# Performance work log

Measured on AMD Instinct MI355X. Metric: run time of the kernel, lower is better.

Reference implementation:

```python
import jax, jax.numpy as jnp
import numpy as np

EPS = 1e-8


def _entropy_1d(p):
    # entropy() helper with input_as_probabilities=True on a 1-D tensor:
    # clamp to EPS, x*log(x), return -sum
    p_ = jnp.maximum(p, EPS)
    return -jnp.sum(p_ * jnp.log(p_))


def setup_inputs() -> dict:
    key = jax.random.key(0)
    k1, k2 = jax.random.split(key)
    b, n = 65536, 512
    anchors = jax.random.normal(k1, (b, n), dtype=jnp.float32)
    neighbors = jax.random.normal(k2, (b, n), dtype=jnp.float32)
    return {"anchors": anchors, "neighbors": neighbors}


def reference(anchors, neighbors):
    entropy_weight = 2.0
    b, n = anchors.shape

    anchors_prob = jax.nn.softmax(anchors, axis=1)      # [b, n]
    positives_prob = jax.nn.softmax(neighbors, axis=1)  # [b, n]

    # bmm of [b,1,n] x [b,n,1] -> row-wise dot product, shape [b]
    similarity = jnp.einsum('bn,bn->b', anchors_prob, positives_prob)

    # BCELoss(similarity, ones) = -mean(log(sim)); torch clamps log at -100
    consistency_loss = -jnp.mean(jnp.maximum(jnp.log(similarity), -100.0))

    lg_sim = jnp.log(similarity)

    entropy_loss = _entropy_1d(jnp.mean(anchors_prob, axis=0))

    # cross/second-order: dot of clamped sim with clamped log-sim
    second_order_loss = jnp.dot(jnp.maximum(similarity, EPS),
                                jnp.maximum(lg_sim, EPS))

    # np.tile(sim, n).reshape(n, b) then view(b, n, 1): equivalent to the
    # flat [b*n] tiled vector reshaped row-major to [b, n]
    tiled_sim = jnp.tile(similarity, n).reshape(b, n)
    third_order_entropy = jnp.einsum('bn,bn->b', anchors_prob, tiled_sim)
    lg_third = jnp.log(third_order_entropy)
    third_order_loss = jnp.dot(jnp.maximum(third_order_entropy, EPS),
                               jnp.maximum(lg_third, EPS)) / n

    third_weight = 0.5 / np.sqrt(n)
    diff_weight = 0.25 / n

    total_loss = (consistency_loss
                  - entropy_weight * entropy_loss
                  + diff_weight * second_order_loss
                  - third_weight * third_order_loss)
    return (total_loss, consistency_loss, entropy_loss,
            second_order_loss, third_order_loss)
```

## Files before the change

### kernel.cpp

```cpp
#include <hip/hip_runtime.h>
#include <math.h>

#define B_ROWS 65536
#define N_COLS 512
#define EPS 1e-8f
#define NREP 8
#define GRID1 2048
#define GRID2 2048


__global__ __launch_bounds__(256) void scan_pass1(
        const float* __restrict__ A, const float* __restrict__ Bn,
        float* __restrict__ sim, float* __restrict__ colsum,
        float* __restrict__ acc) {
    __shared__ float cs[512];
    __shared__ float sred[8];

    const int t    = threadIdx.x;
    const int lane = t & 63;
    const int sub  = lane & 15;
    const int g    = lane >> 4;
    const int wave = (blockIdx.x * 256 + t) >> 6;

    float cacc[32];
#pragma unroll
    for (int k = 0; k < 32; ++k) cacc[k] = 0.f;
    float accLog = 0.f, accSec = 0.f;

#pragma unroll
    for (int iter = 0; iter < 2; ++iter) {
        const int row = wave * 4 + g + iter * 32768;
        const float* a = A  + (size_t)row * N_COLS;
        const float* b = Bn + (size_t)row * N_COLS;

        float4 av4[8], bv4[8];
#pragma unroll
        for (int k = 0; k < 8; ++k) {
            av4[k] = *(const float4*)(a + (k * 16 + sub) * 4);
            bv4[k] = *(const float4*)(b + (k * 16 + sub) * 4);
        }

        float ea[32];
        float sa = 0.f, sb = 0.f, dp = 0.f;
#pragma unroll
        for (int k = 0; k < 8; ++k) {
            float avv[4] = {av4[k].x, av4[k].y, av4[k].z, av4[k].w};
            float bvv[4] = {bv4[k].x, bv4[k].y, bv4[k].z, bv4[k].w};
#pragma unroll
            for (int c = 0; c < 4; ++c) {
                float e = __expf(avv[c]);
                float f = __expf(bvv[c]);
                ea[k * 4 + c] = e;
                sa += e; sb += f; dp += e * f;
            }
        }

#pragma unroll
        for (int m = 8; m >= 1; m >>= 1) {
            sa += __shfl_xor(sa, m, 64);
            sb += __shfl_xor(sb, m, 64);
            dp += __shfl_xor(dp, m, 64);
        }

        float inv_sa = 1.f / sa;
#pragma unroll
        for (int k = 0; k < 32; ++k) cacc[k] += ea[k] * inv_sa;

        if (sub == 0) {
            float s = dp * inv_sa * (1.f / sb);
            sim[row] = s;
            float lg = __logf(s);
            accLog += fmaxf(lg, -100.f);
            accSec += fmaxf(s, EPS) * fmaxf(lg, EPS);
        }
    }

    accLog += __shfl_xor(accLog, 16, 64); accLog += __shfl_xor(accLog, 32, 64);
    accSec += __shfl_xor(accSec, 16, 64); accSec += __shfl_xor(accSec, 32, 64);

    cs[t] = 0.f; cs[t + 256] = 0.f;
    __syncthreads();
#pragma unroll
    for (int k = 0; k < 8; ++k)
#pragma unroll
        for (int c = 0; c < 4; ++c)
            atomicAdd(&cs[64 * k + 4 * sub + c], cacc[k * 4 + c]);
    if (lane == 0) { sred[(t >> 6)] = accLog; sred[4 + (t >> 6)] = accSec; }
    __syncthreads();

    float* crep = colsum + (blockIdx.x & (NREP - 1)) * 512;
    atomicAdd(&crep[t], cs[t]);
    atomicAdd(&crep[t + 256], cs[t + 256]);
    if (t == 0)
        atomicAdd(&acc[0], sred[0] + sred[1] + sred[2] + sred[3]);
    if (t == 1)
        atomicAdd(&acc[1], sred[4] + sred[5] + sred[6] + sred[7]);
}

__global__ __launch_bounds__(256) void scan_pass2(
        const float* __restrict__ A, const float* __restrict__ sim,
        float* __restrict__ acc) {
    __shared__ float sred[4];
    const int t    = threadIdx.x;
    const int lane = t & 63;
    const int sub  = lane & 15;
    const int g    = lane >> 4;
    const int wave = (blockIdx.x * 256 + t) >> 6;

    const int slab = (wave * 4 + g) & 127;
    const float* sp = sim + (size_t)slab * N_COLS;
    float4 sv4[8];
#pragma unroll
    for (int k = 0; k < 8; ++k)
        sv4[k] = *(const float4*)(sp + (k * 16 + sub) * 4);

    float accThird = 0.f;
#pragma unroll
    for (int iter = 0; iter < 2; ++iter) {
        const int row = wave * 4 + g + iter * 32768;
        const float* a = A + (size_t)row * N_COLS;
        float4 av4[8];
#pragma unroll
        for (int k = 0; k < 8; ++k)
            av4[k] = *(const float4*)(a + (k * 16 + sub) * 4);

        float sa = 0.f, dp = 0.f;
#pragma unroll
        for (int k = 0; k < 8; ++k) {
            float avv[4] = {av4[k].x, av4[k].y, av4[k].z, av4[k].w};
            float svv[4] = {sv4[k].x, sv4[k].y, sv4[k].z, sv4[k].w};
#pragma unroll
            for (int c = 0; c < 4; ++c) {
                float e = __expf(avv[c]);
                sa += e;
                dp += e * svv[c];
            }
        }
#pragma unroll
        for (int m = 8; m >= 1; m >>= 1) {
            sa += __shfl_xor(sa, m, 64);
            dp += __shfl_xor(dp, m, 64);
        }
        if (sub == 0) {
            float toe = dp / sa;
            float lg  = __logf(toe);
            accThird += fmaxf(toe, EPS) * fmaxf(lg, EPS);
        }
    }

    accThird += __shfl_xor(accThird, 16, 64);
    accThird += __shfl_xor(accThird, 32, 64);
    if (lane == 0) sred[t >> 6] = accThird;
    __syncthreads();
    if (t == 0)
        atomicAdd(&acc[2], sred[0] + sred[1] + sred[2] + sred[3]);
}

__global__ __launch_bounds__(64) void scan_finalize(
        const float* __restrict__ colsum, const float* __restrict__ acc,
        float* __restrict__ out) {
    const int lane = threadIdx.x;
    float e = 0.f;
#pragma unroll
    for (int k = 0; k < 8; ++k) {
        const int col = lane * 8 + k;
        float c = 0.f;
#pragma unroll
        for (int r = 0; r < NREP; ++r) c += colsum[r * 512 + col];
        float p = c * (1.f / B_ROWS);
        p = fmaxf(p, EPS);
        e -= p * __logf(p);
    }
#pragma unroll
    for (int m = 32; m >= 1; m >>= 1) e += __shfl_xor(e, m, 64);
    if (lane == 0) {
        float consistency = -acc[0] * (1.f / B_ROWS);
        float second      = acc[1];
        float third       = acc[2] * (1.f / N_COLS);
        float entropy     = e;
        float third_weight = 0.5f / sqrtf((float)N_COLS);
        float diff_weight  = 0.25f / (float)N_COLS;
        float total = consistency - 2.0f * entropy + diff_weight * second
                      - third_weight * third;
        out[0] = total;
        out[1] = consistency;
        out[2] = entropy;
        out[3] = second;
        out[4] = third;
    }
}

extern "C" void kernel_launch(void* const* d_in, const int* in_sizes, int n_in,
                              void* d_out, int out_size, void* d_ws, size_t ws_size,
                              hipStream_t stream) {
    const float* anchors   = (const float*)d_in[0];
    const float* neighbors = (const float*)d_in[1];
    float* out = (float*)d_out;

    float* sim    = (float*)d_ws;
    float* colsum = sim + B_ROWS;
    float* acc    = colsum + NREP * 512;

    hipMemsetAsync(colsum, 0, (NREP * 512 + 4) * sizeof(float), stream);

    scan_pass1<<<dim3(GRID1), dim3(256), 0, stream>>>(anchors, neighbors, sim, colsum, acc);
    scan_pass2<<<dim3(GRID2), dim3(256), 0, stream>>>(anchors, sim, acc);
    scan_finalize<<<1, 64, 0, stream>>>(colsum, acc, out);
}
```

Measured before the change: 350.9 us.

## Materialize anchor softmax as bf16 in pass 1 and reuse it in pass 2

```diff
diff --git a/kernel.cpp b/kernel.cpp
--- a/kernel.cpp
+++ b/kernel.cpp
@@ -9,151 +9,250 @@
 #define GRID2 2048
 
 
-__global__ __launch_bounds__(256) void scan_pass1(
+__device__ __forceinline__ unsigned int pack_bf16_2(float lo, float hi) {
+    unsigned int ulo = __float_as_uint(lo);
+    unsigned int uhi = __float_as_uint(hi);
+    ulo = (ulo + 0x7FFFu + ((ulo >> 16) & 1u)) >> 16;
+    uhi = (uhi + 0x7FFFu + ((uhi >> 16) & 1u)) & 0xFFFF0000u;
+    return ulo | uhi;
+}
+
+__global__ __launch_bounds__(256) void k1_sims(
         const float* __restrict__ A, const float* __restrict__ Bn,
-        float* __restrict__ sim, float* __restrict__ colsum,
-        float* __restrict__ acc) {
-    __shared__ float cs[512];
+        float* __restrict__ sim, unsigned int* __restrict__ Pb,
+        float* __restrict__ acc, int storeP) {
     __shared__ float sred[8];
-
     const int t    = threadIdx.x;
     const int lane = t & 63;
-    const int sub  = lane & 15;
-    const int g    = lane >> 4;
     const int wave = (blockIdx.x * 256 + t) >> 6;
 
-    float cacc[32];
-#pragma unroll
-    for (int k = 0; k < 32; ++k) cacc[k] = 0.f;
     float accLog = 0.f, accSec = 0.f;
 
 #pragma unroll
-    for (int iter = 0; iter < 2; ++iter) {
-        const int row = wave * 4 + g + iter * 32768;
-        const float* a = A  + (size_t)row * N_COLS;
-        const float* b = Bn + (size_t)row * N_COLS;
-
-        float4 av4[8], bv4[8];
-#pragma unroll
-        for (int k = 0; k < 8; ++k) {
-            av4[k] = *(const float4*)(a + (k * 16 + sub) * 4);
-            bv4[k] = *(const float4*)(b + (k * 16 + sub) * 4);
-        }
-
-        float ea[32];
-        float sa = 0.f, sb = 0.f, dp = 0.f;
-#pragma unroll
-        for (int k = 0; k < 8; ++k) {
-            float avv[4] = {av4[k].x, av4[k].y, av4[k].z, av4[k].w};
-            float bvv[4] = {bv4[k].x, bv4[k].y, bv4[k].z, bv4[k].w};
-#pragma unroll
-            for (int c = 0; c < 4; ++c) {
-                float e = __expf(avv[c]);
-                float f = __expf(bvv[c]);
-                ea[k * 4 + c] = e;
-                sa += e; sb += f; dp += e * f;
-            }
-        }
-
-#pragma unroll
-        for (int m = 8; m >= 1; m >>= 1) {
-            sa += __shfl_xor(sa, m, 64);
-            sb += __shfl_xor(sb, m, 64);
-            dp += __shfl_xor(dp, m, 64);
-        }
-
-        float inv_sa = 1.f / sa;
-#pragma unroll
-        for (int k = 0; k < 32; ++k) cacc[k] += ea[k] * inv_sa;
-
-        if (sub == 0) {
-            float s = dp * inv_sa * (1.f / sb);
-            sim[row] = s;
-            float lg = __logf(s);
-            accLog += fmaxf(lg, -100.f);
-            accSec += fmaxf(s, EPS) * fmaxf(lg, EPS);
-        }
-    }
-
-    accLog += __shfl_xor(accLog, 16, 64); accLog += __shfl_xor(accLog, 32, 64);
-    accSec += __shfl_xor(accSec, 16, 64); accSec += __shfl_xor(accSec, 32, 64);
+    for (int batch = 0; batch < 2; ++batch) {
+        float4 a0[4], a1[4], b0[4], b1[4];
+#pragma unroll
+        for (int q = 0; q < 4; ++q) {
+            const int row = wave + (q + batch * 4) * 8192;
+            const float* a = A  + (size_t)row * N_COLS;
+            const float* b = Bn + (size_t)row * N_COLS;
+            a0[q] = *(const float4*)(a + lane * 4);
+            a1[q] = *(const float4*)(a + 256 + lane * 4);
+            b0[q] = *(const float4*)(b + lane * 4);
+            b1[q] = *(const float4*)(b + 256 + lane * 4);
+        }
+        float ea[4][8], sa[4], sb[4], dp[4];
+#pragma unroll
+        for (int q = 0; q < 4; ++q) {
+            float av[8] = {a0[q].x, a0[q].y, a0[q].z, a0[q].w,
+                           a1[q].x, a1[q].y, a1[q].z, a1[q].w};
+            float bv[8] = {b0[q].x, b0[q].y, b0[q].z, b0[q].w,
+                           b1[q].x, b1[q].y, b1[q].z, b1[q].w};
+            float s = 0.f, sB = 0.f, d = 0.f;
+#pragma unroll
+            for (int k = 0; k < 8; ++k) {
+                float e = __expf(av[k]);
+                float f = __expf(bv[k]);
+                ea[q][k] = e;
+                s += e; sB += f; d += e * f;
+            }
+            sa[q] = s; sb[q] = sB; dp[q] = d;
+        }
+#pragma unroll
+        for (int m = 32; m >= 1; m >>= 1) {
+#pragma unroll
+            for (int q = 0; q < 4; ++q) {
+                sa[q] += __shfl_xor(sa[q], m, 64);
+                sb[q] += __shfl_xor(sb[q], m, 64);
+                dp[q] += __shfl_xor(dp[q], m, 64);
+            }
+        }
+#pragma unroll
+        for (int q = 0; q < 4; ++q) {
+            const int row = wave + (q + batch * 4) * 8192;
+            float inv_sa = 1.f / sa[q];
+            float s = dp[q] * inv_sa * (1.f / sb[q]);
+            if (lane == 0) {
+                sim[row] = s;
+                float lg = __logf(s);
+                accLog += fmaxf(lg, -100.f);
+                accSec += fmaxf(s, EPS) * fmaxf(lg, EPS);
+            }
+            if (storeP) {
+                float p[8];
+#pragma unroll
+                for (int k = 0; k < 8; ++k) p[k] = ea[q][k] * inv_sa;
+                uint2 wlo, whi;
+                wlo.x = pack_bf16_2(p[0], p[1]);
+                wlo.y = pack_bf16_2(p[2], p[3]);
+                whi.x = pack_bf16_2(p[4], p[5]);
+                whi.y = pack_bf16_2(p[6], p[7]);
+                unsigned int* pr = Pb + (size_t)row * 256;
+                *(uint2*)(pr + lane * 2)       = wlo;
+                *(uint2*)(pr + 128 + lane * 2) = whi;
+            }
+        }
+    }
+
+    if (lane == 0) { sred[t >> 6] = accLog; sred[4 + (t >> 6)] = accSec; }
+    __syncthreads();
+    if (t == 0) atomicAdd(&acc[0], sred[0] + sred[1] + sred[2] + sred[3]);
+    if (t == 1) atomicAdd(&acc[1], sred[4] + sred[5] + sred[6] + sred[7]);
+}
+
+__global__ __launch_bounds__(256) void k2_fromP(
+        const unsigned int* __restrict__ Pb, const float* __restrict__ sim,
+        float* __restrict__ colsum, float* __restrict__ acc) {
+    __shared__ float cs[512];
+    __shared__ float sred[4];
+    const int t    = threadIdx.x;
+    const int lane = t & 63;
+    const int wave = (blockIdx.x * 256 + t) >> 6;
+
+    const float* sp = sim + (size_t)(wave & 127) * N_COLS;
+    float4 sv0 = *(const float4*)(sp + lane * 4);
+    float4 sv1 = *(const float4*)(sp + 256 + lane * 4);
+    const float sv[8] = {sv0.x, sv0.y, sv0.z, sv0.w, sv1.x, sv1.y, sv1.z, sv1.w};
+
+    float cacc[8];
+#pragma unroll
+    for (int k = 0; k < 8; ++k) cacc[k] = 0.f;
+    float accThird = 0.f;
+
+#pragma unroll
+    for (int batch = 0; batch < 2; ++batch) {
+        uint2 wlo[4], whi[4];
+#pragma unroll
+        for (int q = 0; q < 4; ++q) {
+            const int row = wave + (q + batch * 4) * 8192;
+            const unsigned int* pr = Pb + (size_t)row * 256;
+            wlo[q] = *(const uint2*)(pr + lane * 2);
+            whi[q] = *(const uint2*)(pr + 128 + lane * 2);
+        }
+        float dp[4];
+#pragma unroll
+        for (int q = 0; q < 4; ++q) {
+            float p[8];
+            p[0] = __uint_as_float(wlo[q].x << 16);
+            p[1] = __uint_as_float(wlo[q].x & 0xFFFF0000u);
+            p[2] = __uint_as_float(wlo[q].y << 16);
+            p[3] = __uint_as_float(wlo[q].y & 0xFFFF0000u);
+            p[4] = __uint_as_float(whi[q].x << 16);
+            p[5] = __uint_as_float(whi[q].x & 0xFFFF0000u);
+            p[6] = __uint_as_float(whi[q].y << 16);
+            p[7] = __uint_as_float(whi[q].y & 0xFFFF0000u);
+            float d = 0.f;
+#pragma unroll
+            for (int k = 0; k < 8; ++k) {
+                cacc[k] += p[k];
+                d += p[k] * sv[k];
+            }
+            dp[q] = d;
+        }
+#pragma unroll
+        for (int m = 32; m >= 1; m >>= 1)
+#pragma unroll
+            for (int q = 0; q < 4; ++q) dp[q] += __shfl_xor(dp[q], m, 64);
+        if (lane == 0) {
+#pragma unroll
+            for (int q = 0; q < 4; ++q) {
+                float toe = dp[q];
+                float lg  = __logf(toe);
+                accThird += fmaxf(toe, EPS) * fmaxf(lg, EPS);
+            }
+        }
+    }
 
     cs[t] = 0.f; cs[t + 256] = 0.f;
     __syncthreads();
 #pragma unroll
-    for (int k = 0; k < 8; ++k)
-#pragma unroll
-        for (int c = 0; c < 4; ++c)
-            atomicAdd(&cs[64 * k + 4 * sub + c], cacc[k * 4 + c]);
-    if (lane == 0) { sred[(t >> 6)] = accLog; sred[4 + (t >> 6)] = accSec; }
-    __syncthreads();
-
+    for (int k = 0; k < 4; ++k) atomicAdd(&cs[lane * 4 + k], cacc[k]);
+#pragma unroll
+    for (int k = 0; k < 4; ++k) atomicAdd(&cs[256 + lane * 4 + k], cacc[4 + k]);
+    if (lane == 0) sred[t >> 6] = accThird;
+    __syncthreads();
     float* crep = colsum + (blockIdx.x & (NREP - 1)) * 512;
     atomicAdd(&crep[t], cs[t]);
     atomicAdd(&crep[t + 256], cs[t + 256]);
-    if (t == 0)
-        atomicAdd(&acc[0], sred[0] + sred[1] + sred[2] + sred[3]);
-    if (t == 1)
-        atomicAdd(&acc[1], sred[4] + sred[5] + sred[6] + sred[7]);
-}
-
-__global__ __launch_bounds__(256) void scan_pass2(
+    if (t == 0) atomicAdd(&acc[2], sred[0] + sred[1] + sred[2] + sred[3]);
+}
+
+__global__ __launch_bounds__(256) void k2_direct(
         const float* __restrict__ A, const float* __restrict__ sim,
-        float* __restrict__ acc) {
+        float* __restrict__ colsum, float* __restrict__ acc) {
+    __shared__ float cs[512];
     __shared__ float sred[4];
     const int t    = threadIdx.x;
     const int lane = t & 63;
-    const int sub  = lane & 15;
-    const int g    = lane >> 4;
     const int wave = (blockIdx.x * 256 + t) >> 6;
 
-    const int slab = (wave * 4 + g) & 127;
-    const float* sp = sim + (size_t)slab * N_COLS;
-    float4 sv4[8];
-#pragma unroll
-    for (int k = 0; k < 8; ++k)
-        sv4[k] = *(const float4*)(sp + (k * 16 + sub) * 4);
-
+    const float* sp = sim + (size_t)(wave & 127) * N_COLS;
+    float4 sv0 = *(const float4*)(sp + lane * 4);
+    float4 sv1 = *(const float4*)(sp + 256 + lane * 4);
+    const float sv[8] = {sv0.x, sv0.y, sv0.z, sv0.w, sv1.x, sv1.y, sv1.z, sv1.w};
+
+    float cacc[8];
+#pragma unroll
+    for (int k = 0; k < 8; ++k) cacc[k] = 0.f;
     float accThird = 0.f;
-#pragma unroll
-    for (int iter = 0; iter < 2; ++iter) {
-        const int row = wave * 4 + g + iter * 32768;
-        const float* a = A + (size_t)row * N_COLS;
-        float4 av4[8];
-#pragma unroll
-        for (int k = 0; k < 8; ++k)
-            av4[k] = *(const float4*)(a + (k * 16 + sub) * 4);
-
-        float sa = 0.f, dp = 0.f;
-#pragma unroll
-        for (int k = 0; k < 8; ++k) {
-            float avv[4] = {av4[k].x, av4[k].y, av4[k].z, av4[k].w};
-            float svv[4] = {sv4[k].x, sv4[k].y, sv4[k].z, sv4[k].w};
-#pragma unroll
-            for (int c = 0; c < 4; ++c) {
-                float e = __expf(avv[c]);
-                sa += e;
-                dp += e * svv[c];
-            }
-        }
-#pragma unroll
-        for (int m = 8; m >= 1; m >>= 1) {
-            sa += __shfl_xor(sa, m, 64);
-            dp += __shfl_xor(dp, m, 64);
-        }
-        if (sub == 0) {
-            float toe = dp / sa;
-            float lg  = __logf(toe);
-            accThird += fmaxf(toe, EPS) * fmaxf(lg, EPS);
-        }
-    }
-
-    accThird += __shfl_xor(accThird, 16, 64);
-    accThird += __shfl_xor(accThird, 32, 64);
+
+#pragma unroll
+    for (int batch = 0; batch < 2; ++batch) {
+        float4 a0[4], a1[4];
+#pragma unroll
+        for (int q = 0; q < 4; ++q) {
+            const int row = wave + (q + batch * 4) * 8192;
+            const float* a = A + (size_t)row * N_COLS;
+            a0[q] = *(const float4*)(a + lane * 4);
+            a1[q] = *(const float4*)(a + 256 + lane * 4);
+        }
+        float ea[4][8], sa[4], dp[4];
+#pragma unroll
+        for (int q = 0; q < 4; ++q) {
+            float av[8] = {a0[q].x, a0[q].y, a0[q].z, a0[q].w,
+                           a1[q].x, a1[q].y, a1[q].z, a1[q].w};
+            float s = 0.f, d = 0.f;
+#pragma unroll
+            for (int k = 0; k < 8; ++k) {
+                float e = __expf(av[k]);
+                ea[q][k] = e;
+                s += e;
+                d += e * sv[k];
+            }
+            sa[q] = s; dp[q] = d;
+        }
+#pragma unroll
+        for (int m = 32; m >= 1; m >>= 1)
+#pragma unroll
+            for (int q = 0; q < 4; ++q) {
+                sa[q] += __shfl_xor(sa[q], m, 64);
+                dp[q] += __shfl_xor(dp[q], m, 64);
+            }
+#pragma unroll
+        for (int q = 0; q < 4; ++q) {
+            float inv_sa = 1.f / sa[q];
+#pragma unroll
+            for (int k = 0; k < 8; ++k) cacc[k] += ea[q][k] * inv_sa;
+            if (lane == 0) {
+                float toe = dp[q] * inv_sa;
+                float lg  = __logf(toe);
+                accThird += fmaxf(toe, EPS) * fmaxf(lg, EPS);
+            }
+        }
+    }
+
+    cs[t] = 0.f; cs[t + 256] = 0.f;
+    __syncthreads();
+#pragma unroll
+    for (int k = 0; k < 4; ++k) atomicAdd(&cs[lane * 4 + k], cacc[k]);
+#pragma unroll
+    for (int k = 0; k < 4; ++k) atomicAdd(&cs[256 + lane * 4 + k], cacc[4 + k]);
     if (lane == 0) sred[t >> 6] = accThird;
     __syncthreads();
-    if (t == 0)
-        atomicAdd(&acc[2], sred[0] + sred[1] + sred[2] + sred[3]);
+    float* crep = colsum + (blockIdx.x & (NREP - 1)) * 512;
+    atomicAdd(&crep[t], cs[t]);
+    atomicAdd(&crep[t + 256], cs[t + 256]);
+    if (t == 0) atomicAdd(&acc[2], sred[0] + sred[1] + sred[2] + sred[3]);
 }
 
 __global__ __launch_bounds__(64) void scan_finalize(
@@ -200,10 +299,18 @@
     float* sim    = (float*)d_ws;
     float* colsum = sim + B_ROWS;
     float* acc    = colsum + NREP * 512;
-
-    hipMemsetAsync(colsum, 0, (NREP * 512 + 4) * sizeof(float), stream);
-
-    scan_pass1<<<dim3(GRID1), dim3(256), 0, stream>>>(anchors, neighbors, sim, colsum, acc);
-    scan_pass2<<<dim3(GRID2), dim3(256), 0, stream>>>(anchors, sim, acc);
+    unsigned int* Pb = (unsigned int*)(acc + 16);
+    const size_t need = (size_t)(B_ROWS + NREP * 512 + 16) * 4
+                      + (size_t)B_ROWS * N_COLS * 2;
+    const int haveP = (ws_size >= need) ? 1 : 0;
+
+    hipMemsetAsync(colsum, 0, (NREP * 512 + 16) * sizeof(float), stream);
+
+    k1_sims<<<dim3(GRID1), dim3(256), 0, stream>>>(
+        anchors, neighbors, sim, Pb, acc, haveP);
+    if (haveP)
+        k2_fromP<<<dim3(GRID2), dim3(256), 0, stream>>>(Pb, sim, colsum, acc);
+    else
+        k2_direct<<<dim3(GRID2), dim3(256), 0, stream>>>(anchors, sim, colsum, acc);
     scan_finalize<<<1, 64, 0, stream>>>(colsum, acc, out);
 }
```

Measured after the change: 333.8 us. -4.9%, faster.
